# Kernel optimization log

Hardware: AMD Instinct MI355X
Metric: run time of the kernel (lower is better)

Reference implementation:

```python
import jax, jax.numpy as jnp
import numpy as np

B, S, D = 4, 4096, 1024
EPS_LN = 1e-5
EPS_REC = 1e-8


def _layernorm(x, g, b):
    mu = jnp.mean(x, axis=-1, keepdims=True)
    var = jnp.mean((x - mu) ** 2, axis=-1, keepdims=True)
    return (x - mu) * jax.lax.rsqrt(var + EPS_LN) * g + b


def setup_inputs() -> dict:
    key = jax.random.key(0)
    ks = jax.random.split(key, 8)
    scale = 1.0 / np.sqrt(D)
    return {
        "x": jax.random.normal(ks[0], (B, S, D), dtype=jnp.float32),
        "x_prev": jax.random.normal(ks[1], (B, S, D), dtype=jnp.float32),
        "mu": jnp.float32(0.5),
        "decay_w": jax.random.uniform(ks[2], (D, 1), jnp.float32, -scale, scale),
        "decay_b": jnp.zeros((1,), jnp.float32),
        "ln1_g": jnp.ones((D,), jnp.float32),
        "ln1_b": jnp.zeros((D,), jnp.float32),
        "Wr_w": jax.random.uniform(ks[3], (D, D), jnp.float32, -scale, scale),
        "Wr_b": jnp.zeros((D,), jnp.float32),
        "Wv_w": jax.random.uniform(ks[4], (D, D), jnp.float32, -scale, scale),
        "Wv_b": jnp.zeros((D,), jnp.float32),
        "ln2_g": jnp.ones((D,), jnp.float32),
        "ln2_b": jnp.zeros((D,), jnp.float32),
    }


def reference(x, x_prev, mu, decay_w, decay_b, ln1_g, ln1_b,
              Wr_w, Wr_b, Wv_w, Wv_b, ln2_g, ln2_b):
    # Shift (token-mix by scalar mu)
    shifted = mu * x + (1.0 - mu) * x_prev  # [B,S,D]

    # SequenceMergingSeq with C = V = W = shifted
    decay = jax.nn.sigmoid(jnp.einsum("bsd,do->bso", shifted, decay_w) + decay_b)  # [B,S,1]
    e = jnp.exp(shifted)                       # [B,S,D]
    ea = jnp.sum(e, axis=-1, keepdims=True)    # [B,S,1]
    ev = e * shifted                           # [B,S,D]

    def step(carry, inp):
        a, b = carry
        d_t, ea_t, ev_t = inp
        a = d_t * a + ea_t            # [B,1]
        b = d_t * b + ev_t            # [B,D]
        return (a, b), b / (a + EPS_REC)

    init = (jnp.zeros((B, 1), shifted.dtype), jnp.zeros((B, D), shifted.dtype))
    xs = (jnp.swapaxes(decay, 0, 1), jnp.swapaxes(ea, 0, 1), jnp.swapaxes(ev, 0, 1))
    _, out_sbd = jax.lax.scan(step, init, xs)  # [S,B,D]
    merged = _layernorm(jnp.swapaxes(out_sbd, 0, 1), ln1_g, ln1_b)  # [B,S,D]

    # StateCoupling
    gate = jax.nn.sigmoid(jnp.einsum("bsd,ed->bse", merged, Wr_w) + Wr_b)
    value = jnp.einsum("bsd,ed->bse", merged, Wv_w) + Wv_b
    coupled = _layernorm(gate * value, ln2_g, ln2_b)

    return shifted + coupled
```

## Files before the change

kernel.cpp:

```cpp
#include <hip/hip_runtime.h>

#define BATCH 4
#define SEQ   4096
#define DIM   1024
#define NCH   512
#define CHK   8
#define NROWS (BATCH*SEQ)
#define NTG   16
#define NPAIR 8

typedef __attribute__((ext_vector_type(4))) float f32x4;
typedef __attribute__((ext_vector_type(8))) short shortx8;
typedef __attribute__((ext_vector_type(4))) short shortx4;

static __device__ __forceinline__ unsigned short f2bf(float f){
    unsigned int u = __float_as_uint(f);
    u += 0x7FFFu + ((u >> 16) & 1u);
    return (unsigned short)(u >> 16);
}
static __device__ __forceinline__ float bf2f(unsigned short h){
    return __uint_as_float(((unsigned int)h) << 16);
}
static __device__ __forceinline__ float sigmoidf_fast(float x){
    return 1.0f / (1.0f + __expf(-x));
}
static __device__ __forceinline__ shortx4 pack4(f32x4 s){
    shortx4 o;
    o.x = (short)f2bf(s.x); o.y = (short)f2bf(s.y);
    o.z = (short)f2bf(s.z); o.w = (short)f2bf(s.w);
    return o;
}
static __device__ __forceinline__ f32x4 unpack4(shortx4 s){
    f32x4 o;
    o.x = bf2f((unsigned short)s.x); o.y = bf2f((unsigned short)s.y);
    o.z = bf2f((unsigned short)s.z); o.w = bf2f((unsigned short)s.w);
    return o;
}

__global__ __launch_bounds__(256) void k_shift_scan(
    const float* __restrict__ X, const float* __restrict__ XP,
    const float* __restrict__ mu_p, const float* __restrict__ dw,
    const float* __restrict__ db_p,
    const float* __restrict__ Wr, const float* __restrict__ Wv,
    unsigned short* __restrict__ Wcat,
    unsigned short* __restrict__ shifted,
    unsigned short* __restrict__ b_local, float* __restrict__ a_local,
    float* __restrict__ cumP)
{
    const int tid  = threadIdx.x;

    if (blockIdx.x >= 512){
        const int pb = blockIdx.x - 512;
        #pragma unroll 4
        for (int i = 0; i < 32; ++i){
            const int n = pb*32 + i;
            const int grp = n >> 5, r = n & 31;
            const float* src = (r < 16) ? (Wr + (size_t)(grp*16 + r)*DIM)
                                        : (Wv + (size_t)(grp*16 + (r-16))*DIM);
            f32x4 v = reinterpret_cast<const f32x4*>(src)[tid];
            reinterpret_cast<shortx4*>(Wcat)[n*256 + tid] = pack4(v);
        }
        return;
    }

    const int lane = tid & 63;
    const int wid  = tid >> 6;
    const int cid  = blockIdx.x*4 + wid;
    const int batch = cid >> 9;
    const int chunk = cid & (NCH-1);
    const int row0  = batch*SEQ + chunk*CHK;

    const float mu = mu_p[0];
    const float om = 1.0f - mu;
    const float db = db_p[0];

    const f32x4* dwv = reinterpret_cast<const f32x4*>(dw);
    const f32x4 w0 = dwv[lane], w1 = dwv[64+lane], w2 = dwv[128+lane], w3 = dwv[192+lane];

    f32x4 b0 = {0,0,0,0}, b1 = {0,0,0,0}, b2 = {0,0,0,0}, b3 = {0,0,0,0};
    float a_run = 0.f, cp = 1.f;

    const f32x4* Xv  = reinterpret_cast<const f32x4*>(X);
    const f32x4* XPv = reinterpret_cast<const f32x4*>(XP);
    shortx4* BL = reinterpret_cast<shortx4*>(b_local);
    shortx4* SH = reinterpret_cast<shortx4*>(shifted);

    for (int r = 0; r < CHK; ++r){
        const int row = row0 + r;
        const int rb  = row*(DIM/4);

        f32x4 x0 = Xv[rb+lane],     x1 = Xv[rb+64+lane],
              x2 = Xv[rb+128+lane], x3 = Xv[rb+192+lane];
        f32x4 p0 = XPv[rb+lane],     p1 = XPv[rb+64+lane],
              p2 = XPv[rb+128+lane], p3 = XPv[rb+192+lane];
        f32x4 s0 = mu*x0 + om*p0, s1 = mu*x1 + om*p1;
        f32x4 s2 = mu*x2 + om*p2, s3 = mu*x3 + om*p3;

        SH[rb+lane]     = pack4(s0);
        SH[rb+64+lane]  = pack4(s1);
        SH[rb+128+lane] = pack4(s2);
        SH[rb+192+lane] = pack4(s3);

        float dot = s0.x*w0.x + s0.y*w0.y + s0.z*w0.z + s0.w*w0.w
                  + s1.x*w1.x + s1.y*w1.y + s1.z*w1.z + s1.w*w1.w
                  + s2.x*w2.x + s2.y*w2.y + s2.z*w2.z + s2.w*w2.w
                  + s3.x*w3.x + s3.y*w3.y + s3.z*w3.z + s3.w*w3.w;

        f32x4 e0, e1, e2, e3;
        e0.x=__expf(s0.x); e0.y=__expf(s0.y); e0.z=__expf(s0.z); e0.w=__expf(s0.w);
        e1.x=__expf(s1.x); e1.y=__expf(s1.y); e1.z=__expf(s1.z); e1.w=__expf(s1.w);
        e2.x=__expf(s2.x); e2.y=__expf(s2.y); e2.z=__expf(s2.z); e2.w=__expf(s2.w);
        e3.x=__expf(s3.x); e3.y=__expf(s3.y); e3.z=__expf(s3.z); e3.w=__expf(s3.w);
        float ea = e0.x+e0.y+e0.z+e0.w + e1.x+e1.y+e1.z+e1.w
                 + e2.x+e2.y+e2.z+e2.w + e3.x+e3.y+e3.z+e3.w;

        #pragma unroll
        for (int off = 1; off < 64; off <<= 1){
            dot += __shfl_xor(dot, off, 64);
            ea  += __shfl_xor(ea,  off, 64);
        }

        const float dt = sigmoidf_fast(dot + db);
        a_run = dt*a_run + ea;
        cp   *= dt;
        b0 = dt*b0 + e0*s0;  b1 = dt*b1 + e1*s1;
        b2 = dt*b2 + e2*s2;  b3 = dt*b3 + e3*s3;

        BL[rb+lane]     = pack4(b0);
        BL[rb+64+lane]  = pack4(b1);
        BL[rb+128+lane] = pack4(b2);
        BL[rb+192+lane] = pack4(b3);
        if (lane == 0){ a_local[row] = a_run; cumP[row] = cp; }
    }
}

__global__ __launch_bounds__(64) void k_combine(
    const unsigned short* __restrict__ b_local, const float* __restrict__ a_local,
    const float* __restrict__ cumP,
    float* __restrict__ carryA, unsigned short* __restrict__ carryB)
{
    const int batch = blockIdx.x >> 2;
    const int dseg  = blockIdx.x & 3;
    const int tid = threadIdx.x;
    const int d0 = dseg*256 + tid*4;

    __shared__ float sP[NCH], sA[NCH];
    for (int c = tid; c < NCH; c += 64){
        const int er = batch*SEQ + c*CHK + (CHK-1);
        sP[c] = cumP[er];
        sA[c] = a_local[er];
    }
    __syncthreads();

    const unsigned short* bl = b_local + (size_t)batch*SEQ*DIM + d0;
    unsigned short* cB = carryB + (size_t)batch*NCH*DIM + d0;
    const bool wA = (dseg == 0 && tid == 0);
    float* cAp = carryA + batch*NCH;

    shortx4 pf[16];
    #pragma unroll
    for (int i = 0; i < 16; ++i)
        pf[i] = *reinterpret_cast<const shortx4*>(bl + (i*CHK + CHK-1)*DIM);

    f32x4 cb = {0,0,0,0};
    float ca = 0.f;

    for (int cc = 0; cc < NCH; cc += 16){
        const bool more = (cc + 16 < NCH);
        #pragma unroll
        for (int k = 0; k < 16; ++k){
            const int c = cc + k;
            f32x4 v = unpack4(pf[k]);
            if (more)
                pf[k] = *reinterpret_cast<const shortx4*>(bl + ((c+16)*CHK + CHK-1)*DIM);
            *reinterpret_cast<shortx4*>(cB + (size_t)c*DIM) = pack4(cb);
            if (wA) cAp[c] = ca;
            const float p = sP[c];
            cb = p*cb + v;
            ca = p*ca + sA[c];
        }
    }
}

__global__ __launch_bounds__(256) void k_fix_ln1(
    const unsigned short* __restrict__ b_local, const float* __restrict__ a_local,
    const float* __restrict__ cumP, const float* __restrict__ carryA,
    const unsigned short* __restrict__ carryB,
    const float* __restrict__ g1, const float* __restrict__ bb1,
    unsigned short* __restrict__ merged)
{
    const int tid = threadIdx.x, lane = tid & 63, wid = tid >> 6;
    const int row = blockIdx.x*4 + wid;
    const int batch = row >> 12;
    const int c = (row & (SEQ-1)) >> 3;

    const float cpv = cumP[row];
    const float a = a_local[row] + cpv * carryA[batch*NCH + c];
    const float inv_a = 1.0f / (a + 1e-8f);

    const shortx4* BL = reinterpret_cast<const shortx4*>(b_local) + (size_t)row*256;
    const shortx4* CB = reinterpret_cast<const shortx4*>(carryB) + (size_t)(batch*NCH + c)*256;

    f32x4 o[4];
    float s = 0.f, s2 = 0.f;
    #pragma unroll
    for (int j = 0; j < 4; ++j){
        f32x4 bl = unpack4(BL[j*64 + lane]);
        f32x4 cb = unpack4(CB[j*64 + lane]);
        f32x4 v = (bl + cpv*cb) * inv_a;
        o[j] = v;
        s  += v.x+v.y+v.z+v.w;
        s2 += v.x*v.x + v.y*v.y + v.z*v.z + v.w*v.w;
    }
    #pragma unroll
    for (int off = 1; off < 64; off <<= 1){
        s  += __shfl_xor(s,  off, 64);
        s2 += __shfl_xor(s2, off, 64);
    }
    const float mean = s * (1.0f/DIM);
    const float rstd = rsqrtf(s2*(1.0f/DIM) - mean*mean + 1e-5f);
    shortx4* MG = reinterpret_cast<shortx4*>(merged) + (size_t)row*256;
    #pragma unroll
    for (int j = 0; j < 4; ++j){
        f32x4 gg = reinterpret_cast<const f32x4*>(g1)[j*64 + lane];
        f32x4 bb = reinterpret_cast<const f32x4*>(bb1)[j*64 + lane];
        MG[j*64 + lane] = pack4((o[j] - mean)*rstd*gg + bb);
    }
}

typedef __attribute__((address_space(3))) unsigned int lds_uint;
typedef __attribute__((address_space(1))) unsigned int glob_uint;
static __device__ __forceinline__ void gload16(const unsigned short* g, char* l){
    __builtin_amdgcn_global_load_lds((const glob_uint*)g, (lds_uint*)l, 16, 0, 0);
}
#define SBAR() do { __builtin_amdgcn_sched_barrier(0); __builtin_amdgcn_s_barrier(); __builtin_amdgcn_sched_barrier(0); } while(0)
#define LGKM0() do { asm volatile("s_waitcnt lgkmcnt(0)" ::: "memory"); __builtin_amdgcn_sched_barrier(0); } while(0)
#define VMC(n)  asm volatile("s_waitcnt vmcnt(" #n ")" ::: "memory")
#define LDSE 136

__global__ __launch_bounds__(512, 2) void k_gemm(
    const unsigned short* __restrict__ A,
    const unsigned short* __restrict__ Bt,
    const float* __restrict__ rbias, const float* __restrict__ vbias,
    unsigned short* __restrict__ gv)
{
    __shared__ __align__(16) char lds[163840];
    const int tid  = threadIdx.x;
    const int lane = tid & 63;
    const int wid  = tid >> 6;
    const int wqm  = wid >> 2;
    const int wqn  = wid & 3;

    const int bid  = blockIdx.x;
    const int wgid = (bid & 7)*64 + (bid >> 3);
    const int mt = wgid >> 3, nt = wgid & 7;
    const int m0 = mt*256, n0 = nt*256;

    const int rin = lane >> 2;
    const int scg = (lane & 3) ^ (((lane >> 5) & 1) << 1);
    const unsigned short* gA = A  + (size_t)(m0 + wid*16 + rin)*DIM + scg*8;
    const unsigned short* gB = Bt + (size_t)(n0 + wid*16 + rin)*DIM + scg*8;

    const int fr = lane & 15, fq = lane >> 4;
    const int soff = fr*64 + ((fq*16) ^ ((fr & 8) ? 32 : 0));

    f32x4 acc0[8], acc1[8], acc2[8], acc3[8];
    #pragma unroll
    for (int i = 0; i < 8; ++i){
        acc0[i] = (f32x4){0,0,0,0}; acc1[i] = (f32x4){0,0,0,0};
        acc2[i] = (f32x4){0,0,0,0}; acc3[i] = (f32x4){0,0,0,0};
    }

    auto STAGE_P = [&](int k){
        if (k >= 4*NTG) return;
        const int T = k >> 2, pc = k & 3, slot = k % 10;
        const int isA = (pc == 0 || pc == 3);
        const int h   = (pc >= 2) ? 1 : 0;
        char* dst = lds + slot*16384 + wid*2048;
        const unsigned short* s = (isA ? gA : gB) + (size_t)(h*128)*DIM + T*64;
        gload16(s,      dst);
        gload16(s + 32, dst + 1024);
    };

    shortx8 aA[8], bB0[4], bB1[4];
    auto LOAD_A = [&](int slot){
        const char* base = lds + slot*16384;
        #pragma unroll
        for (int rf = 0; rf < 4; ++rf)
            #pragma unroll
            for (int kb = 0; kb < 2; ++kb)
                aA[rf*2+kb] = *reinterpret_cast<const shortx8*>(
                    base + (wqm*4 + rf)*2048 + kb*1024 + soff);
    };
    auto LOAD_B = [&](int slot, shortx8* dst){
        const char* base = lds + slot*16384;
        #pragma unroll
        for (int cf = 0; cf < 2; ++cf)
            #pragma unroll
            for (int kb = 0; kb < 2; ++kb)
                dst[cf*2+kb] = *reinterpret_cast<const shortx8*>(
                    base + (wqn*2 + cf)*2048 + kb*1024 + soff);
    };

    #define MFMA16(ACC, BX)                                                     \
        __builtin_amdgcn_s_setprio(1);                                          \
        _Pragma("unroll")                                                       \
        for (int rf = 0; rf < 4; ++rf)                                          \
            _Pragma("unroll")                                                   \
            for (int cf = 0; cf < 2; ++cf){                                     \
                ACC[rf*2+cf] = __builtin_amdgcn_mfma_f32_16x16x32_bf16(         \
                    aA[rf*2+0], BX[cf*2+0], ACC[rf*2+cf], 0,0,0);               \
                ACC[rf*2+cf] = __builtin_amdgcn_mfma_f32_16x16x32_bf16(         \
                    aA[rf*2+1], BX[cf*2+1], ACC[rf*2+cf], 0,0,0);               \
            }                                                                   \
        __builtin_amdgcn_s_setprio(0);

    #pragma unroll
    for (int k = 0; k < 8; ++k) STAGE_P(k);
    VMC(6);
    SBAR();

    for (int i = 0; i < NPAIR; ++i){
        const int T0 = 2*i;
        const int sA0t0 = (4*T0  ) % 10, sB0t0 = (4*T0+1) % 10;
        const int sB1t0 = (4*T0+2) % 10, sA1t0 = (4*T0+3) % 10;
        const int sA0t1 = (4*T0+4) % 10, sB0t1 = (4*T0+5) % 10;
        const int sB1t1 = (4*T0+6) % 10, sA1t1 = (4*T0+7) % 10;
        const int P = 8*i;
        const bool last = (i == NPAIR-1);

        LOAD_A(sA0t0); LOAD_B(sB0t0, bB0);
        STAGE_P(P + 8);
        LGKM0();
        MFMA16(acc0, bB0);
        SBAR();
        LOAD_B(sB1t0, bB1);
        STAGE_P(P + 9);
        LGKM0();
        MFMA16(acc1, bB1);
        SBAR();
        LOAD_A(sA1t0);
        STAGE_P(P + 10);
        LGKM0();
        MFMA16(acc3, bB1);
        SBAR();
        STAGE_P(P + 11);
        if (last) { VMC(0); } else { VMC(6); }
        MFMA16(acc2, bB0);
        SBAR();
        LOAD_A(sA0t1); LOAD_B(sB0t1, bB0);
        STAGE_P(P + 12);
        LGKM0();
        MFMA16(acc0, bB0);
        SBAR();
        LOAD_B(sB1t1, bB1);
        STAGE_P(P + 13);
        LGKM0();
        MFMA16(acc1, bB1);
        SBAR();
        LOAD_A(sA1t1);
        STAGE_P(P + 14);
        LGKM0();
        MFMA16(acc3, bB1);
        SBAR();
        STAGE_P(P + 15);
        if (!last) { VMC(6); }
        MFMA16(acc2, bB0);
        SBAR();
    }

    __syncthreads();
    unsigned short* ep = reinterpret_cast<unsigned short*>(lds);
    #pragma unroll
    for (int q = 0; q < 4; ++q){
        const f32x4* ac = (q==0) ? acc0 : (q==1) ? acc1 : (q==2) ? acc2 : acc3;
        const int QM = q >> 1, QN = q & 1;
        const int el = QN*64 + wqn*16 + fr;
        const float rbe = rbias[nt*128 + el];
        const float vbe = vbias[nt*128 + el];
        #pragma unroll
        for (int rf = 0; rf < 4; ++rf){
            const int rbase = QM*128 + wqm*64 + rf*16 + fq*4;
            f32x4 ga = ac[rf*2+0], va = ac[rf*2+1];
            #pragma unroll
            for (int qq = 0; qq < 4; ++qq){
                const float g = sigmoidf_fast(ga[qq] + rbe);
                ep[(rbase + qq)*LDSE + el] = f2bf(g*(va[qq] + vbe));
            }
        }
    }
    __syncthreads();
    #pragma unroll
    for (int p = 0; p < 8; ++p){
        const int r  = p*32 + (tid >> 4);
        const int c8 = tid & 15;
        shortx8 val = *reinterpret_cast<const shortx8*>(&ep[r*LDSE + c8*8]);
        *reinterpret_cast<shortx8*>(&gv[(size_t)(m0 + r)*DIM + nt*128 + c8*8]) = val;
    }
    #undef MFMA16
}

__global__ __launch_bounds__(256) void k_ln2_res(
    const unsigned short* __restrict__ gvb, const unsigned short* __restrict__ shifted,
    const float* __restrict__ g2, const float* __restrict__ b2,
    float* __restrict__ out)
{
    const int tid = threadIdx.x, lane = tid & 63, wid = tid >> 6;
    const int row = blockIdx.x*4 + wid;

    const shortx4* GV = reinterpret_cast<const shortx4*>(gvb) + (size_t)row*256;
    const shortx4* SH = reinterpret_cast<const shortx4*>(shifted) + (size_t)row*256;

    f32x4 v[4];
    float s = 0.f, s2 = 0.f;
    #pragma unroll
    for (int j = 0; j < 4; ++j){
        f32x4 x = unpack4(GV[j*64 + lane]);
        v[j] = x;
        s  += x.x+x.y+x.z+x.w;
        s2 += x.x*x.x + x.y*x.y + x.z*x.z + x.w*x.w;
    }
    #pragma unroll
    for (int off = 1; off < 64; off <<= 1){
        s  += __shfl_xor(s,  off, 64);
        s2 += __shfl_xor(s2, off, 64);
    }
    const float mean = s * (1.0f/DIM);
    const float rstd = rsqrtf(s2*(1.0f/DIM) - mean*mean + 1e-5f);
    f32x4* O = reinterpret_cast<f32x4*>(out) + (size_t)row*256;
    #pragma unroll
    for (int j = 0; j < 4; ++j){
        f32x4 gg = reinterpret_cast<const f32x4*>(g2)[j*64 + lane];
        f32x4 bb = reinterpret_cast<const f32x4*>(b2)[j*64 + lane];
        f32x4 sh = unpack4(SH[j*64 + lane]);
        O[j*64 + lane] = sh + (v[j] - mean)*rstd*gg + bb;
    }
}

extern "C" void kernel_launch(void* const* d_in, const int* in_sizes, int n_in,
                              void* d_out, int out_size, void* d_ws, size_t ws_size,
                              hipStream_t stream)
{
    (void)in_sizes; (void)n_in; (void)out_size; (void)ws_size;
    const float* x     = (const float*)d_in[0];
    const float* xprev = (const float*)d_in[1];
    const float* mu    = (const float*)d_in[2];
    const float* dw    = (const float*)d_in[3];
    const float* db    = (const float*)d_in[4];
    const float* ln1g  = (const float*)d_in[5];
    const float* ln1b  = (const float*)d_in[6];
    const float* Wr    = (const float*)d_in[7];
    const float* Wrb   = (const float*)d_in[8];
    const float* Wv    = (const float*)d_in[9];
    const float* Wvb   = (const float*)d_in[10];
    const float* ln2g  = (const float*)d_in[11];
    const float* ln2b  = (const float*)d_in[12];
    float* out = (float*)d_out;

    char* ws = (char*)d_ws;
    size_t off = 0;
    auto alloc = [&](size_t bytes) -> void* {
        void* p = ws + off;
        off += (bytes + 255) & ~(size_t)255;
        return p;
    };
    unsigned short* shifted = (unsigned short*)alloc((size_t)NROWS*DIM*2);
    unsigned short* b_local = (unsigned short*)alloc((size_t)NROWS*DIM*2);
    unsigned short* merged  = (unsigned short*)alloc((size_t)NROWS*DIM*2);
    unsigned short* carryB  = (unsigned short*)alloc((size_t)BATCH*NCH*DIM*2);
    unsigned short* Wcat    = (unsigned short*)alloc((size_t)2048*1024*2);
    float* a_local          = (float*)alloc((size_t)NROWS*4);
    float* cumP             = (float*)alloc((size_t)NROWS*4);
    float* carryA           = (float*)alloc((size_t)BATCH*NCH*4);
    unsigned short* gvbuf   = b_local;

    hipLaunchKernelGGL(k_shift_scan, dim3(576),  dim3(256), 0, stream,
                       x, xprev, mu, dw, db, Wr, Wv, Wcat, shifted, b_local, a_local, cumP);
    hipLaunchKernelGGL(k_combine,    dim3(16),   dim3(64),  0, stream,
                       b_local, a_local, cumP, carryA, carryB);
    hipLaunchKernelGGL(k_fix_ln1,    dim3(4096), dim3(256), 0, stream,
                       b_local, a_local, cumP, carryA, carryB, ln1g, ln1b, merged);
    hipLaunchKernelGGL(k_gemm,       dim3(512),  dim3(512), 0, stream,
                       merged, Wcat, Wrb, Wvb, gvbuf);
    hipLaunchKernelGGL(k_ln2_res,    dim3(4096), dim3(256), 0, stream,
                       gvbuf, shifted, ln2g, ln2b, out);
}
```

Baseline: 208.1 us.

## Restructure GEMM main loop to one barrier per K tile

After: 205.0 us. About the same (-1.5%).

```diff
diff --git a/kernel.cpp b/kernel.cpp
--- a/kernel.cpp
+++ b/kernel.cpp
@@ -7,7 +7,6 @@
 #define CHK   8
 #define NROWS (BATCH*SEQ)
 #define NTG   16
-#define NPAIR 8
 
 typedef __attribute__((ext_vector_type(4))) float f32x4;
 typedef __attribute__((ext_vector_type(8))) short shortx8;
@@ -234,8 +233,8 @@
     __builtin_amdgcn_global_load_lds((const glob_uint*)g, (lds_uint*)l, 16, 0, 0);
 }
 #define SBAR() do { __builtin_amdgcn_sched_barrier(0); __builtin_amdgcn_s_barrier(); __builtin_amdgcn_sched_barrier(0); } while(0)
-#define LGKM0() do { asm volatile("s_waitcnt lgkmcnt(0)" ::: "memory"); __builtin_amdgcn_sched_barrier(0); } while(0)
-#define VMC(n)  asm volatile("s_waitcnt vmcnt(" #n ")" ::: "memory")
+#define LGKM(n) do { asm volatile("s_waitcnt lgkmcnt(" #n ")" ::: "memory"); __builtin_amdgcn_sched_barrier(0); } while(0)
+#define VMC(n)  do { asm volatile("s_waitcnt vmcnt(" #n ")" ::: "memory"); __builtin_amdgcn_sched_barrier(0); } while(0)
 #define LDSE 136
 
 __global__ __launch_bounds__(512, 2) void k_gemm(
@@ -316,56 +315,32 @@
         __builtin_amdgcn_s_setprio(0);
 
     #pragma unroll
-    for (int k = 0; k < 8; ++k) STAGE_P(k);
-    VMC(6);
+    for (int k = 0; k < 6; ++k) STAGE_P(k);
+    VMC(4);
     SBAR();
 
-    for (int i = 0; i < NPAIR; ++i){
-        const int T0 = 2*i;
-        const int sA0t0 = (4*T0  ) % 10, sB0t0 = (4*T0+1) % 10;
-        const int sB1t0 = (4*T0+2) % 10, sA1t0 = (4*T0+3) % 10;
-        const int sA0t1 = (4*T0+4) % 10, sB0t1 = (4*T0+5) % 10;
-        const int sB1t1 = (4*T0+6) % 10, sA1t1 = (4*T0+7) % 10;
-        const int P = 8*i;
-        const bool last = (i == NPAIR-1);
-
-        LOAD_A(sA0t0); LOAD_B(sB0t0, bB0);
-        STAGE_P(P + 8);
-        LGKM0();
+    #pragma unroll
+    for (int T = 0; T < NTG; ++T){
+        const int p0 = 4*T;
+        STAGE_P(p0+6); STAGE_P(p0+7); STAGE_P(p0+8); STAGE_P(p0+9);
+
+        const int sA0 = p0 % 10, sB0 = (p0+1) % 10;
+        const int sB1 = (p0+2) % 10, sA1 = (p0+3) % 10;
+
+        LOAD_A(sA0);
+        LOAD_B(sB0, bB0);
+        LOAD_B(sB1, bB1);
+        LGKM(4);
         MFMA16(acc0, bB0);
-        SBAR();
-        LOAD_B(sB1t0, bB1);
-        STAGE_P(P + 9);
-        LGKM0();
+        LGKM(0);
         MFMA16(acc1, bB1);
-        SBAR();
-        LOAD_A(sA1t0);
-        STAGE_P(P + 10);
-        LGKM0();
+        LOAD_A(sA1);
+        LGKM(0);
         MFMA16(acc3, bB1);
-        SBAR();
-        STAGE_P(P + 11);
-        if (last) { VMC(0); } else { VMC(6); }
         MFMA16(acc2, bB0);
-        SBAR();
-        LOAD_A(sA0t1); LOAD_B(sB0t1, bB0);
-        STAGE_P(P + 12);
-        LGKM0();
-        MFMA16(acc0, bB0);
-        SBAR();
-        LOAD_B(sB1t1, bB1);
-        STAGE_P(P + 13);
-        LGKM0();
-        MFMA16(acc1, bB1);
-        SBAR();
-        LOAD_A(sA1t1);
-        STAGE_P(P + 14);
-        LGKM0();
-        MFMA16(acc3, bB1);
-        SBAR();
-        STAGE_P(P + 15);
-        if (!last) { VMC(6); }
-        MFMA16(acc2, bB0);
+
+        if (T < NTG-2)       { VMC(4); }
+        else if (T == NTG-2) { VMC(0); }
         SBAR();
     }
 
```
